# Kernel optimization log

Hardware: AMD Instinct MI355X
Metric: run time of the kernel (lower is better)

The kernel has to match this reference:

```python
import jax, jax.numpy as jnp
import numpy as np

B, T, H, W = 4, 16, 64, 64
NUM_CLASSES = 512
C_OUT = 256
KT, KH, KW = 3, 3, 3


def setup_inputs() -> dict:
    key = jax.random.key(0)
    k1, k2, k3 = jax.random.split(key, 3)
    indices = jax.random.randint(k1, (B, T, H, W), 0, NUM_CLASSES, dtype=jnp.int32)
    weight = jax.random.normal(k2, (C_OUT, NUM_CLASSES, KT, KH, KW), dtype=jnp.float32) * 0.05
    bias = jax.random.normal(k3, (C_OUT,), dtype=jnp.float32) * 0.05
    return {"indices": indices, "weight": weight, "bias": bias}


def reference(indices, weight, bias):
    # indices: [B,T,H,W] int palette ids; weight: [C_out,K,kT,kH,kW]; bias: [C_out]
    kT, kH, kW = weight.shape[2:]
    b, t, h, w = indices.shape
    c_out = weight.shape[0]
    # causal temporal pad (replicate first frame) + spatial replicate pad
    padded = jnp.pad(
        indices,
        ((0, 0), (kT - 1, 0), (kH // 2, kH // 2), (kW // 2, kW // 2)),
        mode="edge",
    )
    acc = jnp.zeros((b, t, h, w, c_out), dtype=weight.dtype)
    # static loop over kernel taps (27); each tap is a per-position weight-row gather
    for dt in range(kT):
        for dh in range(kH):
            for dw in range(kW):
                tap = weight[:, :, dt, dh, dw].T          # [num_classes, C_out]
                idx = padded[:, dt:dt + t, dh:dh + h, dw:dw + w]  # [B,T,H,W]
                acc = acc + tap[idx]                      # gather -> [B,T,H,W,C_out]
    out = acc + bias                                      # broadcast bias over C_out
    return jnp.transpose(out, (0, 4, 1, 2, 3))            # [B,C_out,T,H,W]
```

## Files before the change

### kernel.cpp

```cpp
#include <hip/hip_runtime.h>
#include <hip/hip_fp16.h>

#define NCLS 512
#define COUT 256
#define BB 4
#define TT 16
#define HH 64
#define WW 64

static constexpr size_t TABLE_ELEMS = 27ull * NCLS * COUT;
static constexpr size_t TABLE_BYTES = TABLE_ELEMS * sizeof(__half);

__global__ __launch_bounds__(256) void repack_kernel(const float* __restrict__ w,
                                                     __half* __restrict__ tbl) {
    int n = blockIdx.x;
    int p = threadIdx.x;
    int c = ((p & 7) << 5) + (p >> 3);
    const float* src = w + ((size_t)c * NCLS + n) * 27;
    float v[27];
#pragma unroll
    for (int k = 0; k < 27; ++k) v[k] = src[k];
#pragma unroll
    for (int k = 0; k < 27; ++k)
        tbl[((size_t)k * NCLS + n) * COUT + p] = __float2half(v[k]);
}

__global__ __launch_bounds__(256, 4) void conv_kernel(const int* __restrict__ idx,
                                                      const __half* __restrict__ tbl,
                                                      const float* __restrict__ bias,
                                                      float* __restrict__ out) {
    __shared__ int soff[3 * 3 * 66];
    __shared__ float tile[16 * 256];

    int bid = ((blockIdx.x & 7) << 9) | (blockIdx.x >> 3);
    int h = bid & 63;
    int t = (bid >> 6) & 15;
    int b = bid >> 10;
    int tid = threadIdx.x;

    for (int e = tid; e < 594; e += 256) {
        int tt = e / 198;
        int r  = e - tt * 198;
        int hh = r / 66;
        int ww = r - hh * 66;
        int ts = t + tt - 2; if (ts < 0) ts = 0;
        int hs = h + hh - 1; if (hs < 0) hs = 0; if (hs > 63) hs = 63;
        int ws = ww - 1;     if (ws < 0) ws = 0; if (ws > 63) ws = 63;
        int n = idx[(((b * TT + ts) * HH) + hs) * WW + ws];
        soff[e] = n << 9;
    }
    __syncthreads();

    int lane = tid & 63;
    int wave = tid >> 6;
    int half = lane >> 5;
    int l5   = lane & 31;
    const char* tb = (const char*)tbl + l5 * 16;

    for (int chunk = 0; chunk < 4; ++chunk) {
#pragma unroll
        for (int pr = 0; pr < 2; ++pr) {
            int w16 = (wave << 2) + (pr << 1) + half;
            int w   = (chunk << 4) + w16;
            __half2 a0 = __float2half2_rn(0.0f);
            __half2 a1 = a0, a2 = a0, a3 = a0;
#pragma unroll
            for (int g = 0; g < 3; ++g) {
                int no[9];
#pragma unroll
                for (int i = 0; i < 9; ++i) {
                    int kt = g * 3 + i / 3;
                    int dw = i % 3;
                    no[i] = soff[kt * 66 + w + dw];
                }
                uint4 ld[9];
#pragma unroll
                for (int i = 0; i < 9; ++i) {
                    int k = g * 9 + i;
                    ld[i] = *reinterpret_cast<const uint4*>(tb + (no[i] + k * 262144));
                }
#pragma unroll
                for (int i = 0; i < 9; ++i) {
                    union { uint4 u; __half2 h2[4]; } v; v.u = ld[i];
                    a0 = __hadd2(a0, v.h2[0]);
                    a1 = __hadd2(a1, v.h2[1]);
                    a2 = __hadd2(a2, v.h2[2]);
                    a3 = __hadd2(a3, v.h2[3]);
                }
            }
            float2 f0 = __half22float2(a0);
            float2 f1 = __half22float2(a1);
            float2 f2 = __half22float2(a2);
            float2 f3 = __half22float2(a3);
            float* tw = &tile[w16 * 256 + l5];
            tw[0]   = f0.x; tw[32]  = f0.y;
            tw[64]  = f1.x; tw[96]  = f1.y;
            tw[128] = f2.x; tw[160] = f2.y;
            tw[192] = f3.x; tw[224] = f3.y;
        }
        __syncthreads();

        {
            int c = tid;
            float bv = bias[c];
            float* obase = out + ((((size_t)b * COUT + c) * TT + t) * HH + h) * WW
                               + (chunk << 4);
#pragma unroll
            for (int q = 0; q < 4; ++q) {
                float4 v;
                v.x = tile[(q * 4 + 0) * 256 + c] + bv;
                v.y = tile[(q * 4 + 1) * 256 + c] + bv;
                v.z = tile[(q * 4 + 2) * 256 + c] + bv;
                v.w = tile[(q * 4 + 3) * 256 + c] + bv;
                *reinterpret_cast<float4*>(obase + q * 4) = v;
            }
        }
        __syncthreads();
    }
}

__global__ __launch_bounds__(256) void conv_direct(const int* __restrict__ idx,
                                                   const float* __restrict__ wgt,
                                                   const float* __restrict__ bias,
                                                   float* __restrict__ out) {
    int bid = blockIdx.x;
    int w = bid & 63;
    int h = (bid >> 6) & 63;
    int t = (bid >> 12) & 15;
    int b = bid >> 16;
    int c = threadIdx.x;
    float acc = bias[c];
#pragma unroll
    for (int dt = 0; dt < 3; ++dt)
#pragma unroll
        for (int dh = 0; dh < 3; ++dh)
#pragma unroll
            for (int dw = 0; dw < 3; ++dw) {
                int ts = t + dt - 2; if (ts < 0) ts = 0;
                int hs = h + dh - 1; if (hs < 0) hs = 0; if (hs > 63) hs = 63;
                int ws = w + dw - 1; if (ws < 0) ws = 0; if (ws > 63) ws = 63;
                int n = idx[(((b * TT + ts) * HH) + hs) * WW + ws];
                acc += wgt[((size_t)(c * NCLS + n)) * 27 + (dt * 9 + dh * 3 + dw)];
            }
    out[((((size_t)b * COUT + c) * TT + t) * HH + h) * WW + w] = acc;
}

extern "C" void kernel_launch(void* const* d_in, const int* in_sizes, int n_in,
                              void* d_out, int out_size, void* d_ws, size_t ws_size,
                              hipStream_t stream) {
    const int*   indices = (const int*)d_in[0];
    const float* weight  = (const float*)d_in[1];
    const float* bias    = (const float*)d_in[2];
    float*       out     = (float*)d_out;

    if (ws_size >= TABLE_BYTES) {
        __half* tbl = (__half*)d_ws;
        repack_kernel<<<NCLS, 256, 0, stream>>>(weight, tbl);
        conv_kernel<<<BB * TT * HH, 256, 0, stream>>>(indices, tbl, bias, out);
    } else {
        conv_direct<<<BB * TT * HH * WW, 256, 0, stream>>>(indices, weight, bias, out);
    }
}
```

Before: 544.8 us.

## Split conv over output-channel halves, stage repack through LDS, use nontemporal stores

The conv kernel now handles 128 output channels per block across a full 64-wide row, and the grid doubles so each position row is covered by two channel-half blocks. This removes the per-chunk barrier loop, leaving one tile write followed by one store phase. The repack kernel loads four classes' worth of weights for 128 channels into shared memory with coalesced reads, then writes half2 pairs, replacing the strided 27-float reads per thread. Output writes use nontemporal float4 stores. In exchange the index-offset staging is duplicated across the two channel halves, and the larger LDS tile may limit occupancy.

```diff
diff --git a/kernel.cpp b/kernel.cpp
--- a/kernel.cpp
+++ b/kernel.cpp
@@ -8,21 +8,48 @@
 #define HH 64
 #define WW 64
 
+typedef float vfloat4 __attribute__((ext_vector_type(4)));
+
 static constexpr size_t TABLE_ELEMS = 27ull * NCLS * COUT;
 static constexpr size_t TABLE_BYTES = TABLE_ELEMS * sizeof(__half);
 
+#define RST 109
+
 __global__ __launch_bounds__(256) void repack_kernel(const float* __restrict__ w,
                                                      __half* __restrict__ tbl) {
-    int n = blockIdx.x;
-    int p = threadIdx.x;
-    int c = ((p & 7) << 5) + (p >> 3);
-    const float* src = w + ((size_t)c * NCLS + n) * 27;
-    float v[27];
+    __shared__ float s[128 * RST];
+
+    int bid  = blockIdx.x;
+    int pass = bid >> 7;
+    int n0   = (bid & 127) << 2;
+    int tid  = threadIdx.x;
+
+    {
+        int r  = tid >> 1;
+        int l2 = tid & 1;
+        int cg = pass * 128 + r;
+        const float* src = w + ((size_t)cg * NCLS + n0) * 27;
 #pragma unroll
-    for (int k = 0; k < 27; ++k) v[k] = src[k];
+        for (int i = 0; i < 54; ++i) {
+            int f = l2 + (i << 1);
+            s[r * RST + f] = src[f];
+        }
+    }
+    __syncthreads();
+
+    unsigned int* tb32 = reinterpret_cast<unsigned int*>(tbl);
+    int n  = tid >> 6;
+    int pd = tid & 63;
+    int c0 = ((pd & 3) << 5) + (pd >> 2);
+    int q0 = n * 27;
 #pragma unroll
-    for (int k = 0; k < 27; ++k)
-        tbl[((size_t)k * NCLS + n) * COUT + p] = __float2half(v[k]);
+    for (int k = 0; k < 27; ++k) {
+        float a = s[c0 * RST + q0 + k];
+        float b = s[(c0 + 16) * RST + q0 + k];
+        __half2 hv = __floats2half2_rn(a, b);
+        tb32[((size_t)k * NCLS + n0 + n) * 128 + pass * 64 + pd] =
+            *reinterpret_cast<unsigned int*>(&hv);
+    }
 }
 
 __global__ __launch_bounds__(256, 4) void conv_kernel(const int* __restrict__ idx,
@@ -30,12 +57,14 @@
                                                       const float* __restrict__ bias,
                                                       float* __restrict__ out) {
     __shared__ int soff[3 * 3 * 66];
-    __shared__ float tile[16 * 256];
+    __shared__ float tile[64 * 136];
 
-    int bid = ((blockIdx.x & 7) << 9) | (blockIdx.x >> 3);
-    int h = bid & 63;
-    int t = (bid >> 6) & 15;
-    int b = bid >> 10;
+    int bx   = blockIdx.x;
+    int pass = (bx >> 2) & 1;
+    int pos  = ((bx & 3) << 10) | (bx >> 3);
+    int h = pos & 63;
+    int t = (pos >> 6) & 15;
+    int b = pos >> 10;
     int tid = threadIdx.x;
 
     for (int e = tid; e < 594; e += 256) {
@@ -53,69 +82,67 @@
 
     int lane = tid & 63;
     int wave = tid >> 6;
-    int half = lane >> 5;
-    int l5   = lane & 31;
-    const char* tb = (const char*)tbl + l5 * 16;
+    int quad = lane >> 4;
+    int l4   = lane & 15;
+    const char* tb = (const char*)tbl + pass * 256 + l4 * 16;
 
-    for (int chunk = 0; chunk < 4; ++chunk) {
 #pragma unroll
-        for (int pr = 0; pr < 2; ++pr) {
-            int w16 = (wave << 2) + (pr << 1) + half;
-            int w   = (chunk << 4) + w16;
-            __half2 a0 = __float2half2_rn(0.0f);
-            __half2 a1 = a0, a2 = a0, a3 = a0;
+    for (int pr = 0; pr < 4; ++pr) {
+        int w = (wave << 4) + (pr << 2) + quad;
+        __half2 a0 = __float2half2_rn(0.0f);
+        __half2 a1 = a0, a2 = a0, a3 = a0;
 #pragma unroll
-            for (int g = 0; g < 3; ++g) {
-                int no[9];
+        for (int g = 0; g < 3; ++g) {
+            int no[9];
 #pragma unroll
-                for (int i = 0; i < 9; ++i) {
-                    int kt = g * 3 + i / 3;
-                    int dw = i % 3;
-                    no[i] = soff[kt * 66 + w + dw];
-                }
-                uint4 ld[9];
+            for (int i = 0; i < 9; ++i) {
+                int kt = g * 3 + i / 3;
+                int dw = i % 3;
+                no[i] = soff[kt * 66 + w + dw];
+            }
+            uint4 ld[9];
 #pragma unroll
-                for (int i = 0; i < 9; ++i) {
-                    int k = g * 9 + i;
-                    ld[i] = *reinterpret_cast<const uint4*>(tb + (no[i] + k * 262144));
-                }
+            for (int i = 0; i < 9; ++i) {
+                int k = g * 9 + i;
+                ld[i] = *reinterpret_cast<const uint4*>(tb + (no[i] + k * 262144));
+            }
 #pragma unroll
-                for (int i = 0; i < 9; ++i) {
-                    union { uint4 u; __half2 h2[4]; } v; v.u = ld[i];
-                    a0 = __hadd2(a0, v.h2[0]);
-                    a1 = __hadd2(a1, v.h2[1]);
-                    a2 = __hadd2(a2, v.h2[2]);
-                    a3 = __hadd2(a3, v.h2[3]);
-                }
-            }
-            float2 f0 = __half22float2(a0);
-            float2 f1 = __half22float2(a1);
-            float2 f2 = __half22float2(a2);
-            float2 f3 = __half22float2(a3);
-            float* tw = &tile[w16 * 256 + l5];
-            tw[0]   = f0.x; tw[32]  = f0.y;
-            tw[64]  = f1.x; tw[96]  = f1.y;
-            tw[128] = f2.x; tw[160] = f2.y;
-            tw[192] = f3.x; tw[224] = f3.y;
-        }
-        __syncthreads();
-
-        {
-            int c = tid;
-            float bv = bias[c];
-            float* obase = out + ((((size_t)b * COUT + c) * TT + t) * HH + h) * WW
-                               + (chunk << 4);
-#pragma unroll
-            for (int q = 0; q < 4; ++q) {
-                float4 v;
-                v.x = tile[(q * 4 + 0) * 256 + c] + bv;
-                v.y = tile[(q * 4 + 1) * 256 + c] + bv;
-                v.z = tile[(q * 4 + 2) * 256 + c] + bv;
-                v.w = tile[(q * 4 + 3) * 256 + c] + bv;
-                *reinterpret_cast<float4*>(obase + q * 4) = v;
+            for (int i = 0; i < 9; ++i) {
+                union { uint4 u; __half2 h2[4]; } v; v.u = ld[i];
+                a0 = __hadd2(a0, v.h2[0]);
+                a1 = __hadd2(a1, v.h2[1]);
+                a2 = __hadd2(a2, v.h2[2]);
+                a3 = __hadd2(a3, v.h2[3]);
             }
         }
-        __syncthreads();
+        float2 f0 = __half22float2(a0);
+        float2 f1 = __half22float2(a1);
+        float2 f2 = __half22float2(a2);
+        float2 f3 = __half22float2(a3);
+        float* tw = &tile[w * 136 + l4];
+        tw[0]   = f0.x; tw[16]  = f0.y;
+        tw[32]  = f1.x; tw[48]  = f1.y;
+        tw[64]  = f2.x; tw[80]  = f2.y;
+        tw[96]  = f3.x; tw[112] = f3.y;
+    }
+    __syncthreads();
+
+    {
+        int c    = tid & 127;
+        int part = tid >> 7;
+        float bv = bias[pass * 128 + c];
+        float* obase = out + ((((size_t)b * COUT + pass * 128 + c) * TT + t) * HH + h) * WW
+                           + part * 32;
+#pragma unroll
+        for (int j = 0; j < 8; ++j) {
+            int w0 = part * 32 + j * 4;
+            vfloat4 v;
+            v.x = tile[(w0 + 0) * 136 + c] + bv;
+            v.y = tile[(w0 + 1) * 136 + c] + bv;
+            v.z = tile[(w0 + 2) * 136 + c] + bv;
+            v.w = tile[(w0 + 3) * 136 + c] + bv;
+            __builtin_nontemporal_store(v, reinterpret_cast<vfloat4*>(obase + j * 4));
+        }
     }
 }
 
@@ -155,8 +182,8 @@
 
     if (ws_size >= TABLE_BYTES) {
         __half* tbl = (__half*)d_ws;
-        repack_kernel<<<NCLS, 256, 0, stream>>>(weight, tbl);
-        conv_kernel<<<BB * TT * HH, 256, 0, stream>>>(indices, tbl, bias, out);
+        repack_kernel<<<256, 256, 0, stream>>>(weight, tbl);
+        conv_kernel<<<2 * BB * TT * HH, 256, 0, stream>>>(indices, tbl, bias, out);
     } else {
         conv_direct<<<BB * TT * HH * WW, 256, 0, stream>>>(indices, weight, bias, out);
     }
```

Result: slower. 986.3 us (+81.0%).
